# Kernel optimization log

Hardware: AMD Instinct MI355X
Metric: run time of the kernel (lower is better)

The kernel has to match this reference:

```python
import jax, jax.numpy as jnp
import numpy as np

D_MODEL = 1024
N_HEADS = 16
D_K = D_MODEL // N_HEADS
SEQ = 2048
BATCH = 2
THETA = 10000.0


def _rope(x, token_positions):
    # x: [b, h, s, dk]; token_positions: [s] int
    k = jnp.arange(0, D_K, 2, dtype=jnp.float32)
    freqs = 1.0 / (THETA ** (k / D_K))                    # [dk/2]
    angles = token_positions.astype(jnp.float32)[:, None] * freqs[None, :]  # [s, dk/2]
    cos = jnp.cos(angles)
    sin = jnp.sin(angles)
    x1 = x[..., 0::2]
    x2 = x[..., 1::2]
    r1 = x1 * cos - x2 * sin
    r2 = x1 * sin + x2 * cos
    out = jnp.stack([r1, r2], axis=-1)                    # [b,h,s,dk/2,2]
    return out.reshape(x.shape)


def setup_inputs() -> dict:
    key = jax.random.key(0)
    ks = jax.random.split(key, 5)
    sigma = np.sqrt(2.0 / (D_MODEL + D_MODEL))
    x = jax.random.normal(ks[0], (BATCH, SEQ, D_MODEL), dtype=jnp.float32)
    Wq = jax.random.truncated_normal(ks[1], -3.0, 3.0, (D_MODEL, D_MODEL), dtype=jnp.float32) * sigma
    Wk = jax.random.truncated_normal(ks[2], -3.0, 3.0, (D_MODEL, D_MODEL), dtype=jnp.float32) * sigma
    Wv = jax.random.truncated_normal(ks[3], -3.0, 3.0, (D_MODEL, D_MODEL), dtype=jnp.float32) * sigma
    Wo = jax.random.truncated_normal(ks[4], -3.0, 3.0, (D_MODEL, D_MODEL), dtype=jnp.float32) * sigma
    token_positions = jnp.arange(SEQ, dtype=jnp.int64)
    return {"x": x, "Wq": Wq, "Wk": Wk, "Wv": Wv, "Wo": Wo, "token_positions": token_positions}


def reference(x, Wq, Wk, Wv, Wo, token_positions):
    b, s, d = x.shape
    # projections: Linear stores weight [out,in], applies x @ W.T
    Q = x @ Wq.T
    K = x @ Wk.T
    V = x @ Wv.T
    # [b, s, h*dk] -> [b, h, s, dk]
    def split_heads(t):
        return t.reshape(b, s, N_HEADS, D_K).transpose(0, 2, 1, 3)
    Q, K, V = split_heads(Q), split_heads(K), split_heads(V)
    Q = _rope(Q, token_positions)
    K = _rope(K, token_positions)
    scale = 1.0 / np.sqrt(D_K).astype(np.float32)
    scores = jnp.einsum('bhqd,bhkd->bhqk', Q, K) * scale   # [b,h,s,s]
    causal = jnp.tril(jnp.ones((s, s), dtype=bool))
    scores = jnp.where(causal, scores, -jnp.inf)
    attn = jax.nn.softmax(scores, axis=-1)
    out = jnp.einsum('bhqk,bhkd->bhqd', attn, V)           # [b,h,s,dk]
    out = out.transpose(0, 2, 1, 3).reshape(b, s, d)
    return out @ Wo.T
```

## Files before the change

kernel.cpp:

```cpp
#include <hip/hip_runtime.h>
#include <hip/hip_bf16.h>
#include <stdint.h>

#define SEQL   2048
#define NBATCH 2
#define BSZ    4096
#define DMODEL 1024
#define NH     16
#define DK     64
#define NBH    32
#define NCHUNK_TOT 40

typedef __attribute__((ext_vector_type(8)))  short short8;
typedef __attribute__((ext_vector_type(4)))  short shortx4;
typedef __attribute__((ext_vector_type(4)))  float f32x4;
typedef __attribute__((ext_vector_type(16))) float f32x16;
typedef __attribute__((ext_vector_type(4)))  unsigned uint4v;
union PU { uint4v u; short8 s; };

__device__ __forceinline__ short f2b(float f) {
  unsigned u = __float_as_uint(f);
  u = (u + 0x7FFF + ((u >> 16) & 1)) >> 16;
  return (short)u;
}
__device__ __forceinline__ float b2f(short s) {
  return __uint_as_float(((unsigned)(unsigned short)s) << 16);
}
__device__ __forceinline__ unsigned cvtpk(float lo, float hi) {
  unsigned r;
  asm("v_cvt_pk_bf16_f32 %0, %1, %2" : "=v"(r) : "v"(lo), "v"(hi));
  return r;
}
#define PLSWAP(a_, b_) asm("v_permlane32_swap_b32 %0, %1" : "+v"(a_), "+v"(b_))

__device__ __forceinline__ void g2l16(const void* g, void* l) {
  __builtin_amdgcn_global_load_lds(
      (__attribute__((address_space(1))) void*)(uintptr_t)g,
      (__attribute__((address_space(3))) void*)l, 16, 0, 0);
}

__device__ __forceinline__ f32x4 mfma16(short8 a, short8 b, f32x4 c) {
  return __builtin_amdgcn_mfma_f32_16x16x32_bf16(a, b, c, 0, 0, 0);
}
__device__ __forceinline__ f32x16 mfma32(short8 a, short8 b, f32x16 c) {
  return __builtin_amdgcn_mfma_f32_32x32x16_bf16(a, b, c, 0, 0, 0);
}

__global__ void cvt_all(const float* __restrict__ x,  const float* __restrict__ wq,
                        const float* __restrict__ wk, const float* __restrict__ wv,
                        const float* __restrict__ wo, short* __restrict__ xb,
                        short* __restrict__ wqkv, short* __restrict__ wob) {
  long idx = ((long)blockIdx.x * 256 + threadIdx.x) * 4;
  const float* s; short* d; long off;
  if (idx < 4194304L)      { s = x;  d = xb;             off = idx; }
  else if (idx < 5242880L) { s = wq; d = wqkv;           off = idx - 4194304L; }
  else if (idx < 6291456L) { s = wk; d = wqkv + 1048576; off = idx - 5242880L; }
  else if (idx < 7340032L) { s = wv; d = wqkv + 2097152; off = idx - 6291456L; }
  else                     { s = wo; d = wob;            off = idx - 7340032L; }
  float4 v = *(const float4*)(s + off);
  shortx4 r;
  r[0] = f2b(v.x); r[1] = f2b(v.y); r[2] = f2b(v.z); r[3] = f2b(v.w);
  *(shortx4*)(d + off) = r;
}

__global__ __launch_bounds__(512, 1)
void gemm256(const short* __restrict__ A, const short* __restrict__ B,
             short* __restrict__ C) {
  __shared__ short As[2][2][8192];
  __shared__ short Bs[2][2][8192];
  int id = blockIdx.x;
  int swz = (id & 7) * 24 + (id >> 3);
  int bm = swz / 12, bn = swz % 12;
  int brow = bm << 8, bcol = bn << 8;
  int tid = threadIdx.x, w = tid >> 6, l = tid & 63;
  int wm = w >> 2, wn = w & 3;
  int lr = l & 15, lg = l >> 4;
  const short* Abase = A + (long)brow * 1024;
  const short* Bbase = B + (long)bcol * 1024;

  f32x4 acc[8][4];
#pragma unroll
  for (int mi = 0; mi < 8; ++mi)
#pragma unroll
    for (int ni = 0; ni < 4; ++ni) acc[mi][ni] = (f32x4){0.f, 0.f, 0.f, 0.f};

#define STGH(srcbase_, kt_, dst_) do {                                          \
    _Pragma("unroll")                                                           \
    for (int i_ = 0; i_ < 2; ++i_) {                                            \
      int idx_ = i_ * 512 + tid;                                                \
      int r_ = idx_ >> 3, gch_ = (idx_ & 7) ^ (r_ & 7);                         \
      g2l16((srcbase_) + (long)r_ * 1024 + (kt_) * 64 + gch_ * 8,               \
            &(dst_)[idx_ * 8]);                                                 \
    } } while (0)

  STGH(Abase,          0, As[0][0]); STGH(Abase + 131072, 0, As[0][1]);
  STGH(Bbase,          0, Bs[0][0]); STGH(Bbase + 131072, 0, Bs[0][1]);
  STGH(Abase,          1, As[1][0]); STGH(Abase + 131072, 1, As[1][1]);
  STGH(Bbase,          1, Bs[1][0]); STGH(Bbase + 131072, 1, Bs[1][1]);
  asm volatile("s_waitcnt vmcnt(8)" ::: "memory");
  __builtin_amdgcn_s_barrier();

  int brw = (wn & 1) * 64;
  for (int kt = 0; kt < 16; ++kt) {
    int cur = kt & 1;
    const short* Ah = &As[cur][wm][0];
    const short* Bh = &Bs[cur][wn >> 1][0];
    short8 a0[4][2], a1[4][2], bf[4][2];
#pragma unroll
    for (int mi = 0; mi < 4; ++mi)
#pragma unroll
      for (int ks = 0; ks < 2; ++ks)
        a0[mi][ks] = *(const short8*)
            &Ah[(mi * 16 + lr) * 64 + (((ks * 4 + lg) ^ (lr & 7)) << 3)];
#pragma unroll
    for (int ni = 0; ni < 4; ++ni)
#pragma unroll
      for (int ks = 0; ks < 2; ++ks)
        bf[ni][ks] = *(const short8*)
            &Bh[(brw + ni * 16 + lr) * 64 + (((ks * 4 + lg) ^ (lr & 7)) << 3)];
    asm volatile("s_waitcnt lgkmcnt(0)" ::: "memory");
    __builtin_amdgcn_sched_barrier(0);
    __builtin_amdgcn_s_setprio(1);
#pragma unroll
    for (int mi = 0; mi < 4; ++mi)
#pragma unroll
      for (int ni = 0; ni < 2; ++ni)
#pragma unroll
        for (int ks = 0; ks < 2; ++ks)
          acc[mi][ni] = mfma16(a0[mi][ks], bf[ni][ks], acc[mi][ni]);
    __builtin_amdgcn_s_setprio(0);
    __builtin_amdgcn_s_barrier();
#pragma unroll
    for (int mi = 0; mi < 4; ++mi)
#pragma unroll
      for (int ks = 0; ks < 2; ++ks)
        a1[mi][ks] = *(const short8*)
            &Ah[((mi + 4) * 16 + lr) * 64 + (((ks * 4 + lg) ^ (lr & 7)) << 3)];
    __builtin_amdgcn_s_setprio(1);
#pragma unroll
    for (int mi = 0; mi < 4; ++mi)
#pragma unroll
      for (int ni = 2; ni < 4; ++ni)
#pragma unroll
        for (int ks = 0; ks < 2; ++ks)
          acc[mi][ni] = mfma16(a0[mi][ks], bf[ni][ks], acc[mi][ni]);
    __builtin_amdgcn_s_setprio(0);
    asm volatile("s_waitcnt lgkmcnt(0)" ::: "memory");
    __builtin_amdgcn_s_barrier();
    if (kt + 2 < 16) {
      STGH(Abase,          kt + 2, As[cur][0]);
      STGH(Abase + 131072, kt + 2, As[cur][1]);
    }
    __builtin_amdgcn_s_setprio(1);
#pragma unroll
    for (int mi = 0; mi < 4; ++mi)
#pragma unroll
      for (int ni = 0; ni < 2; ++ni)
#pragma unroll
        for (int ks = 0; ks < 2; ++ks)
          acc[mi + 4][ni] = mfma16(a1[mi][ks], bf[ni][ks], acc[mi + 4][ni]);
    __builtin_amdgcn_s_setprio(0);
    __builtin_amdgcn_s_barrier();
    if (kt + 2 < 16) {
      STGH(Bbase,          kt + 2, Bs[cur][0]);
      STGH(Bbase + 131072, kt + 2, Bs[cur][1]);
    }
    __builtin_amdgcn_s_setprio(1);
#pragma unroll
    for (int mi = 0; mi < 4; ++mi)
#pragma unroll
      for (int ni = 2; ni < 4; ++ni)
#pragma unroll
        for (int ks = 0; ks < 2; ++ks)
          acc[mi + 4][ni] = mfma16(a1[mi][ks], bf[ni][ks], acc[mi + 4][ni]);
    __builtin_amdgcn_s_setprio(0);
    if (kt + 1 < 16) {
      if (kt + 2 < 16) asm volatile("s_waitcnt vmcnt(8)" ::: "memory");
      else             asm volatile("s_waitcnt vmcnt(0)" ::: "memory");
    }
    __builtin_amdgcn_s_barrier();
  }
#undef STGH

#pragma unroll
  for (int mi = 0; mi < 8; ++mi)
#pragma unroll
    for (int ni = 0; ni < 4; ++ni)
#pragma unroll
      for (int rr = 0; rr < 4; ++rr) {
        int grow = brow + wm * 128 + mi * 16 + lg * 4 + rr;
        int gcol = bcol + wn * 64 + ni * 16 + lr;
        int mat = gcol >> 10, cin = gcol & 1023;
        C[(long)mat * 4194304 + (long)grow * 1024 + cin] = f2b(acc[mi][ni][rr]);
      }
}

template<int CBF16>
__global__ __launch_bounds__(256, 2)
void gemm_bt(const short* __restrict__ A, const short* __restrict__ B,
             void* __restrict__ Cv, int M, int N, int K,
             long bStride, long cStride) {
  __shared__ short As[2][4096];
  __shared__ short Bs[2][4096];
  B += (long)blockIdx.y * bStride;
  int nbn = N >> 7;
  int bm = blockIdx.x / nbn, bn = blockIdx.x % nbn;
  int tid = threadIdx.x, w = tid >> 6, l = tid & 63;
  int wm = w >> 1, wn = w & 1;
  int lr = l & 15, lg = l >> 4;
  int brow = bm << 7, bcol = bn << 7;

  const f32x4 fz = {0.f, 0.f, 0.f, 0.f};
  f32x4 acc[4][4];
#pragma unroll
  for (int xi = 0; xi < 4; ++xi)
#pragma unroll
    for (int yi = 0; yi < 4; ++yi) acc[xi][yi] = fz;

#define GSTAGE(k0_, bi_) do {                                                   \
    _Pragma("unroll")                                                           \
    for (int i_ = 0; i_ < 2; ++i_) {                                            \
      int c_ = w * 2 + i_;                                                      \
      int chunk_ = c_ * 64 + l;                                                 \
      int row_ = chunk_ >> 2, ch_ = chunk_ & 3;                                 \
      int gch_ = ch_ ^ ((row_ >> 1) & 3);                                       \
      g2l16(A + (long)(brow + row_) * K + (k0_) + gch_ * 8, &As[bi_][c_ * 512]);\
      g2l16(B + (long)(bcol + row_) * K + (k0_) + gch_ * 8, &Bs[bi_][c_ * 512]);\
    }                                                                           \
  } while (0)

  GSTAGE(0, 0);
  for (int k0 = 0; k0 < K; k0 += 32) {
    int cb = (k0 >> 5) & 1;
    if (k0 + 32 < K) {
      GSTAGE(k0 + 32, cb ^ 1);
      asm volatile("s_waitcnt vmcnt(4)" ::: "memory");
    } else {
      asm volatile("s_waitcnt vmcnt(0)" ::: "memory");
    }
    __builtin_amdgcn_s_barrier();

    short8 af[4], bfr[4];
#pragma unroll
    for (int xi = 0; xi < 4; ++xi) {
      int ar = wm * 64 + xi * 16 + lr;
      af[xi] = *(const short8*)&As[cb][ar * 32 + ((lg ^ ((ar >> 1) & 3)) << 3)];
      int br = wn * 64 + xi * 16 + lr;
      bfr[xi] = *(const short8*)&Bs[cb][br * 32 + ((lg ^ ((br >> 1) & 3)) << 3)];
    }
    __builtin_amdgcn_s_setprio(1);
#pragma unroll
    for (int xi = 0; xi < 4; ++xi)
#pragma unroll
      for (int yi = 0; yi < 4; ++yi)
        acc[xi][yi] = mfma16(af[xi], bfr[yi], acc[xi][yi]);
    __builtin_amdgcn_s_setprio(0);
    asm volatile("s_waitcnt lgkmcnt(0)" ::: "memory");
    __builtin_amdgcn_s_barrier();
  }
#undef GSTAGE

  if (CBF16) {
    short* Cp = (short*)Cv + (long)blockIdx.y * cStride;
#pragma unroll
    for (int xi = 0; xi < 4; ++xi)
#pragma unroll
      for (int yi = 0; yi < 4; ++yi)
#pragma unroll
        for (int r = 0; r < 4; ++r) {
          int row = brow + wm * 64 + xi * 16 + lg * 4 + r;
          int col = bcol + wn * 64 + yi * 16 + lr;
          Cp[(long)row * N + col] = f2b(acc[xi][yi][r]);
        }
  } else {
    float* Cp = (float*)Cv;
#pragma unroll
    for (int xi = 0; xi < 4; ++xi)
#pragma unroll
      for (int yi = 0; yi < 4; ++yi)
#pragma unroll
        for (int r = 0; r < 4; ++r) {
          int row = brow + wm * 64 + xi * 16 + lg * 4 + r;
          int col = bcol + wn * 64 + yi * 16 + lr;
          Cp[(long)row * N + col] = acc[xi][yi][r];
        }
  }
}

__global__ void rope_split(const short* __restrict__ qkv, const int* __restrict__ tok,
                           short* __restrict__ Qh, short* __restrict__ Kh) {
  int t = blockIdx.x * 256 + threadIdx.x;
  int qd = t & 15, h = (t >> 4) & 15, bs = t >> 8;
  int b = bs >> 11, s = bs & 2047;
  float pos = (float)tok[s];
  long srcoff = (long)bs * 1024 + h * 64 + qd * 4;
  shortx4 q4 = *(const shortx4*)(qkv + srcoff);
  shortx4 k4 = *(const shortx4*)(qkv + 4194304L + srcoff);
  shortx4 qo, ko;
#pragma unroll
  for (int p = 0; p < 2; ++p) {
    int i = qd * 2 + p;
    float freq = exp2f(-(float)i * (13.287712379549449f / 32.0f));
    float ang = pos * freq;
    float sn, cs;
    sincosf(ang, &sn, &cs);
    const float QS = 0.125f * 1.44269504f;
    float x1 = b2f(q4[p * 2]), x2 = b2f(q4[p * 2 + 1]);
    qo[p * 2]     = f2b((x1 * cs - x2 * sn) * QS);
    qo[p * 2 + 1] = f2b((x1 * sn + x2 * cs) * QS);
    float y1 = b2f(k4[p * 2]), y2 = b2f(k4[p * 2 + 1]);
    ko[p * 2]     = f2b(y1 * cs - y2 * sn);
    ko[p * 2 + 1] = f2b(y1 * sn + y2 * cs);
  }
  long outoff = ((long)(b * 16 + h) * 2048 + s) * 64 + qd * 4;
  *(shortx4*)(Qh + outoff) = qo;
  *(shortx4*)(Kh + outoff) = ko;
}

__global__ void vtrans(const short* __restrict__ Vlin, short* __restrict__ Vt) {
  __shared__ short tile[64][72];
  int s0 = blockIdx.x * 64;
  int bh = blockIdx.y;
  int b = bh >> 4, h = bh & 15;
  int t = threadIdx.x;
  int r = t >> 2, c0 = (t & 3) * 16;
  const short* src = Vlin + ((long)(b * 2048 + s0 + r)) * 1024 + h * 64 + c0;
  *(short8*)&tile[r][c0]     = *(const short8*)src;
  *(short8*)&tile[r][c0 + 8] = *(const short8*)(src + 8);
  __syncthreads();
  int d = t >> 2, sc0 = (t & 3) * 16;
  short8 o0, o1;
#pragma unroll
  for (int j = 0; j < 8; ++j) { o0[j] = tile[sc0 + j][d]; o1[j] = tile[sc0 + 8 + j][d]; }
  short* dst = Vt + ((long)(bh * 64 + d)) * 2048 + s0 + sc0;
  *(short8*)dst       = o0;
  *(short8*)(dst + 8) = o1;
}

__global__ __launch_bounds__(256, 3)
void attn_fwd(const short* __restrict__ Qh, const short* __restrict__ Kh,
              const short* __restrict__ Vt, short* __restrict__ poO,
              float* __restrict__ pmb, float* __restrict__ plb) {
  __shared__ short Ks[3][4096];
  __shared__ short Vs[3][4096];
  int bh = blockIdx.x;
  int xr = 39 - blockIdx.y;
  int qi, c = xr, nc = 1;
  for (qi = 0; qi < 16; ++qi) { nc = (qi >> 2) + 1; if (c < nc) break; c -= nc; }
  int n = 2 * qi + 2;
  int t0 = (c * n) / nc, t1 = ((c + 1) * n) / nc;
  int q0b = qi << 7;
  int tid = threadIdx.x, w = tid >> 6, l = tid & 63;
  int ql = l & 31, hi = l >> 5;
  const short* Qb = Qh + (long)bh * (2048 * 64);
  const short* Kb = Kh + (long)bh * (2048 * 64);
  const short* Vb = Vt + (long)bh * (64 * 2048);
  int qw = q0b + 32 * w;
  int qg = qw + ql;
  int pid = bh * NCHUNK_TOT + xr;

  short8 qf[4];
#pragma unroll
  for (int kc = 0; kc < 4; ++kc)
    qf[kc] = *(const short8*)(Qb + (long)qg * 64 + kc * 16 + hi * 8);

  f32x16 o0, o1;
#pragma unroll
  for (int r = 0; r < 16; ++r) { o0[r] = 0.f; o1[r] = 0.f; }
  float m = -1e30f, lsum = 0.f;

#define STAGE(t_, bufi_) do {                                                   \
    int s0_ = (t_) << 6;                                                        \
    _Pragma("unroll")                                                           \
    for (int i_ = 0; i_ < 2; ++i_) {                                            \
      int c_ = w + 4 * i_;                                                      \
      int g_ = c_ >> 2, cc_ = c_ & 3;                                           \
      g2l16(Kb + ((long)(s0_ + g_ * 32 + ql)) * 64 + cc_ * 16 + hi * 8,         \
            &Ks[bufi_][c_ * 512]);                                              \
      g2l16(Vb + ((long)(g_ * 32 + ql)) * 2048 + s0_ + cc_ * 16 + hi * 8,       \
            &Vs[bufi_][c_ * 512]);                                              \
    }                                                                           \
  } while (0)

  STAGE(t0, 0);
  if (t0 + 1 < t1) STAGE(t0 + 1, 1);
  int cur = 0;

  for (int t = t0; t < t1; ++t) {
    if (t + 2 < t1) {
      int nb = cur + 2; if (nb >= 3) nb -= 3;
      STAGE(t + 2, nb);
      asm volatile("s_waitcnt vmcnt(8)" ::: "memory");
    } else if (t + 1 < t1) {
      asm volatile("s_waitcnt vmcnt(4)" ::: "memory");
    } else {
      asm volatile("s_waitcnt vmcnt(0)" ::: "memory");
    }
    __builtin_amdgcn_s_barrier();
    int s0 = t << 6;
    if (s0 <= qw + 31) {
      bool upper = (s0 + 32 <= qw + 31);
      f32x16 sT0, sT1;
#pragma unroll
      for (int r = 0; r < 16; ++r) { sT0[r] = 0.f; sT1[r] = 0.f; }
      __builtin_amdgcn_s_setprio(1);
#pragma unroll
      for (int kc = 0; kc < 4; ++kc) {
        short8 k0 = *(const short8*)&Ks[cur][(kc * 64 + l) * 8];
        sT0 = mfma32(k0, qf[kc], sT0);
      }
      if (upper) {
#pragma unroll
        for (int kc = 0; kc < 4; ++kc) {
          short8 k1 = *(const short8*)&Ks[cur][((4 + kc) * 64 + l) * 8];
          sT1 = mfma32(k1, qf[kc], sT1);
        }
      }
      __builtin_amdgcn_s_setprio(0);
      if (s0 + 63 > qw) {
#pragma unroll
        for (int r = 0; r < 16; ++r) {
          int kvl = (r & 3) + 8 * (r >> 2) + 4 * hi;
          if (s0 + kvl > qg) sT0[r] = -1e30f;
        }
        if (upper) {
#pragma unroll
          for (int r = 0; r < 16; ++r) {
            int kvl = (r & 3) + 8 * (r >> 2) + 4 * hi;
            if (s0 + 32 + kvl > qg) sT1[r] = -1e30f;
          }
        }
      }
      float pmax = sT0[0];
#pragma unroll
      for (int r = 1; r < 16; ++r) pmax = fmaxf(pmax, sT0[r]);
      if (upper) {
#pragma unroll
        for (int r = 0; r < 16; ++r) pmax = fmaxf(pmax, sT1[r]);
      }
      pmax = fmaxf(pmax, __shfl_xor(pmax, 32));
      if (__any(pmax > m + 11.5416f)) {
        float mn = fmaxf(m, pmax);
        float sf = exp2f(m - mn);
        m = mn;
        lsum *= sf;
#pragma unroll
        for (int r = 0; r < 16; ++r) {
          int row = (r & 3) + 8 * (r >> 2) + 4 * hi;
          float fo = __shfl(sf, row);
          o0[r] *= fo; o1[r] *= fo;
        }
      }
      float rs = 0.f;
#pragma unroll
      for (int r = 0; r < 16; ++r) {
        float p = exp2f(sT0[r] - m);
        sT0[r] = p; rs += p;
      }
      if (upper) {
#pragma unroll
        for (int r = 0; r < 16; ++r) {
          float p = exp2f(sT1[r] - m);
          sT1[r] = p; rs += p;
        }
      }
      rs += __shfl_xor(rs, 32);
      lsum += rs;
      short8 pa[4];
      {
        unsigned cA[4], cB[4];
#pragma unroll
        for (int g = 0; g < 4; ++g) {
          cA[g] = cvtpk(sT0[4 * g], sT0[4 * g + 1]);
          cB[g] = cvtpk(sT0[4 * g + 2], sT0[4 * g + 3]);
        }
        PLSWAP(cA[0], cA[1]); PLSWAP(cB[0], cB[1]);
        PLSWAP(cA[2], cA[3]); PLSWAP(cB[2], cB[3]);
        PU p0; p0.u = (uint4v){cA[0], cB[0], cA[1], cB[1]}; pa[0] = p0.s;
        PU p1; p1.u = (uint4v){cA[2], cB[2], cA[3], cB[3]}; pa[1] = p1.s;
      }
      if (upper) {
        unsigned cA[4], cB[4];
#pragma unroll
        for (int g = 0; g < 4; ++g) {
          cA[g] = cvtpk(sT1[4 * g], sT1[4 * g + 1]);
          cB[g] = cvtpk(sT1[4 * g + 2], sT1[4 * g + 3]);
        }
        PLSWAP(cA[0], cA[1]); PLSWAP(cB[0], cB[1]);
        PLSWAP(cA[2], cA[3]); PLSWAP(cB[2], cB[3]);
        PU p2; p2.u = (uint4v){cA[0], cB[0], cA[1], cB[1]}; pa[2] = p2.s;
        PU p3; p3.u = (uint4v){cA[2], cB[2], cA[3], cB[3]}; pa[3] = p3.s;
      }
      __builtin_amdgcn_s_setprio(1);
#pragma unroll
      for (int kc = 0; kc < 2; ++kc) {
        short8 v0 = *(const short8*)&Vs[cur][(kc * 64 + l) * 8];
        short8 v1 = *(const short8*)&Vs[cur][((4 + kc) * 64 + l) * 8];
        o0 = mfma32(pa[kc], v0, o0);
        o1 = mfma32(pa[kc], v1, o1);
      }
      if (upper) {
#pragma unroll
        for (int kc = 2; kc < 4; ++kc) {
          short8 v0 = *(const short8*)&Vs[cur][(kc * 64 + l) * 8];
          short8 v1 = *(const short8*)&Vs[cur][((4 + kc) * 64 + l) * 8];
          o0 = mfma32(pa[kc], v0, o0);
          o1 = mfma32(pa[kc], v1, o1);
        }
      }
      __builtin_amdgcn_s_setprio(0);
    }
    asm volatile("s_waitcnt lgkmcnt(0)" ::: "memory");
    __builtin_amdgcn_s_barrier();
    ++cur; if (cur >= 3) cur -= 3;
  }
#undef STAGE

  if (hi == 0) {
    pmb[pid * 128 + w * 32 + ql] = m;
    plb[pid * 128 + w * 32 + ql] = lsum;
  }
#pragma unroll
  for (int r = 0; r < 16; ++r) {
    int row = (r & 3) + 8 * (r >> 2) + 4 * hi;
    long basep = ((long)pid * 128 + w * 32 + row) * 64;
    poO[basep + ql]      = f2b(o0[r]);
    poO[basep + 32 + ql] = f2b(o1[r]);
  }
}

__global__ void attn_combine(const short* __restrict__ poO,
                             const float* __restrict__ pmb,
                             const float* __restrict__ plb,
                             short* __restrict__ Oh) {
  int x = blockIdx.x, bh = blockIdx.y;
  int qi = x >> 2, sub = x & 3;
  int t = threadIdx.x;
  int r = sub * 32 + (t >> 3);
  int d0 = (t & 7) * 8;
  int nc = (qi >> 2) + 1;
  int prefix = 0;
  for (int j = 0; j < qi; ++j) prefix += (j >> 2) + 1;
  int base = bh * NCHUNK_TOT + prefix;
  float M = -1e30f;
  for (int i = 0; i < nc; ++i)
    M = fmaxf(M, pmb[(base + i) * 128 + r]);
  float acc0 = 0, acc1 = 0, acc2 = 0, acc3 = 0, acc4 = 0, acc5 = 0, acc6 = 0, acc7 = 0;
  float den = 0.f;
  for (int i = 0; i < nc; ++i) {
    float wgt = exp2f(pmb[(base + i) * 128 + r] - M);
    den += wgt * plb[(base + i) * 128 + r];
    short8 ov = *(const short8*)&poO[((long)(base + i) * 128 + r) * 64 + d0];
    acc0 += wgt * b2f(ov[0]); acc1 += wgt * b2f(ov[1]);
    acc2 += wgt * b2f(ov[2]); acc3 += wgt * b2f(ov[3]);
    acc4 += wgt * b2f(ov[4]); acc5 += wgt * b2f(ov[5]);
    acc6 += wgt * b2f(ov[6]); acc7 += wgt * b2f(ov[7]);
  }
  float inv = 1.0f / den;
  int b = bh >> 4, h = bh & 15;
  int s = qi * 128 + r;
  short8 out;
  out[0] = f2b(acc0 * inv); out[1] = f2b(acc1 * inv);
  out[2] = f2b(acc2 * inv); out[3] = f2b(acc3 * inv);
  out[4] = f2b(acc4 * inv); out[5] = f2b(acc5 * inv);
  out[6] = f2b(acc6 * inv); out[7] = f2b(acc7 * inv);
  *(short8*)&Oh[((long)(b * 2048 + s)) * 1024 + h * 64 + d0] = out;
}

extern "C" void kernel_launch(void* const* d_in, const int* in_sizes, int n_in,
                              void* d_out, int out_size, void* d_ws, size_t ws_size,
                              hipStream_t stream) {
  const float* x  = (const float*)d_in[0];
  const float* wq = (const float*)d_in[1];
  const float* wk = (const float*)d_in[2];
  const float* wv = (const float*)d_in[3];
  const float* wo = (const float*)d_in[4];
  const int* tok  = (const int*)d_in[5];

  short* wsp  = (short*)d_ws;
  short* xb   = wsp;
  short* wqkv = xb + 4194304;
  short* wob  = wqkv + 3145728;
  short* qkv  = wob + 1048576;
  short* qh   = qkv + 12582912;
  short* kh   = qh + 4194304;
  short* vt   = kh + 4194304;
  short* oh   = vt + 4194304;

  short* poO = qkv;
  float* pmb = (float*)xb;
  float* plb = pmb + NCHUNK_TOT * NBH * 128;

  (void)in_sizes; (void)n_in; (void)out_size; (void)ws_size;

  cvt_all<<<8192, 256, 0, stream>>>(x, wq, wk, wv, wo, xb, wqkv, wob);
  gemm256<<<192, 512, 0, stream>>>(xb, wqkv, qkv);
  rope_split<<<4096, 256, 0, stream>>>(qkv, tok, qh, kh);
  vtrans<<<dim3(32, 32), 256, 0, stream>>>(qkv + 8388608, vt);
  attn_fwd<<<dim3(32, NCHUNK_TOT), 256, 0, stream>>>(qh, kh, vt, poO, pmb, plb);
  attn_combine<<<dim3(64, 32), 256, 0, stream>>>(poO, pmb, plb, oh);
  gemm_bt<0><<<dim3(256, 1), 256, 0, stream>>>(oh, wob, d_out, 4096, 1024, 1024,
                                               0L, 0L);
}
```

Baseline: 132.7 us.

## Retile QKV GEMM to 256x192 blocks, lighten attention pipelining and row-sum

The QKV projection GEMM moves from 256x256 tiles on 192 blocks to 256x192 tiles on 256 blocks, so every compute unit on the 256-CU part gets a block, with matching changes to the staging and fragment indexing. The attention kernel drops from triple to double buffering of K/V in LDS and raises launch bounds to 4 blocks per CU for more occupancy. It also keeps per-register running sums so the cross-lane row-sum reduction happens once at the end instead of every tile, and uses v_max3 for the row max. The risks are less latency hiding in attention, extra registers for the row sums, and lower per-block arithmetic intensity in the GEMM.

Result: slower. 142.3 us (+7.2%).

```diff
diff --git a/kernel.cpp b/kernel.cpp
--- a/kernel.cpp
+++ b/kernel.cpp
@@ -30,6 +30,11 @@
   unsigned r;
   asm("v_cvt_pk_bf16_f32 %0, %1, %2" : "=v"(r) : "v"(lo), "v"(hi));
   return r;
+}
+__device__ __forceinline__ float max3f(float a, float b, float c) {
+  float d;
+  asm("v_max3_f32 %0, %1, %2, %3" : "=v"(d) : "v"(a), "v"(b), "v"(c));
+  return d;
 }
 #define PLSWAP(a_, b_) asm("v_permlane32_swap_b32 %0, %1" : "+v"(a_), "+v"(b_))
 
@@ -66,58 +71,62 @@
 __global__ __launch_bounds__(512, 1)
 void gemm256(const short* __restrict__ A, const short* __restrict__ B,
              short* __restrict__ C) {
-  __shared__ short As[2][2][8192];
-  __shared__ short Bs[2][2][8192];
+  __shared__ short As[2][16384];
+  __shared__ short Bs[2][12288];
   int id = blockIdx.x;
-  int swz = (id & 7) * 24 + (id >> 3);
-  int bm = swz / 12, bn = swz % 12;
-  int brow = bm << 8, bcol = bn << 8;
-  int tid = threadIdx.x, w = tid >> 6, l = tid & 63;
+  int swz = (id & 7) * 32 + (id >> 3);
+  int bm = swz >> 4, bn = swz & 15;
+  int brow = bm << 8, bcoln = bn * 192;
+  int tid = threadIdx.x, w = tid >> 6;
   int wm = w >> 2, wn = w & 3;
-  int lr = l & 15, lg = l >> 4;
+  int lr = tid & 15, lg = (tid >> 4) & 3;
   const short* Abase = A + (long)brow * 1024;
-  const short* Bbase = B + (long)bcol * 1024;
-
-  f32x4 acc[8][4];
+  const short* Bbase = B + (long)bcoln * 1024;
+
+  f32x4 acc[8][3];
 #pragma unroll
   for (int mi = 0; mi < 8; ++mi)
 #pragma unroll
-    for (int ni = 0; ni < 4; ++ni) acc[mi][ni] = (f32x4){0.f, 0.f, 0.f, 0.f};
-
-#define STGH(srcbase_, kt_, dst_) do {                                          \
-    _Pragma("unroll")                                                           \
-    for (int i_ = 0; i_ < 2; ++i_) {                                            \
-      int idx_ = i_ * 512 + tid;                                                \
-      int r_ = idx_ >> 3, gch_ = (idx_ & 7) ^ (r_ & 7);                         \
-      g2l16((srcbase_) + (long)r_ * 1024 + (kt_) * 64 + gch_ * 8,               \
-            &(dst_)[idx_ * 8]);                                                 \
-    } } while (0)
-
-  STGH(Abase,          0, As[0][0]); STGH(Abase + 131072, 0, As[0][1]);
-  STGH(Bbase,          0, Bs[0][0]); STGH(Bbase + 131072, 0, Bs[0][1]);
-  STGH(Abase,          1, As[1][0]); STGH(Abase + 131072, 1, As[1][1]);
-  STGH(Bbase,          1, Bs[1][0]); STGH(Bbase + 131072, 1, Bs[1][1]);
-  asm volatile("s_waitcnt vmcnt(8)" ::: "memory");
+    for (int ni = 0; ni < 3; ++ni) acc[mi][ni] = (f32x4){0.f, 0.f, 0.f, 0.f};
+
+#define STGA(s_, kt_, buf_) do {                                                \
+    int r_ = tid >> 3, gch_ = (tid & 7) ^ (r_ & 7);                             \
+    g2l16(Abase + (long)((s_) * 64 + r_) * 1024 + (kt_) * 64 + gch_ * 8,        \
+          &As[buf_][(s_) * 4096 + tid * 8]); } while (0)
+#define STGB(s_, kt_, buf_) do {                                                \
+    int r_ = tid >> 3, gch_ = (tid & 7) ^ (r_ & 7);                             \
+    g2l16(Bbase + (long)((s_) * 64 + r_) * 1024 + (kt_) * 64 + gch_ * 8,        \
+          &Bs[buf_][(s_) * 4096 + tid * 8]); } while (0)
+
+  STGA(0,0,0); STGA(1,0,0); STGA(2,0,0); STGA(3,0,0);
+  STGB(0,0,0); STGB(1,0,0); STGB(2,0,0);
+  STGA(0,1,1); STGA(1,1,1); STGA(2,1,1); STGA(3,1,1);
+  STGB(0,1,1); STGB(1,1,1); STGB(2,1,1);
+  asm volatile("s_waitcnt vmcnt(7)" ::: "memory");
   __builtin_amdgcn_s_barrier();
 
-  int brw = (wn & 1) * 64;
   for (int kt = 0; kt < 16; ++kt) {
     int cur = kt & 1;
-    const short* Ah = &As[cur][wm][0];
-    const short* Bh = &Bs[cur][wn >> 1][0];
-    short8 a0[4][2], a1[4][2], bf[4][2];
-#pragma unroll
-    for (int mi = 0; mi < 4; ++mi)
+    const short* Ah = &As[cur][wm * 8192];
+    const short* Bh = &Bs[cur][0];
+    short8 a0[4][2], a1[4][2], bf[3][2];
+#pragma unroll
+    for (int mi = 0; mi < 4; ++mi) {
+      int rin = mi * 16 + lr;
 #pragma unroll
       for (int ks = 0; ks < 2; ++ks)
         a0[mi][ks] = *(const short8*)
-            &Ah[(mi * 16 + lr) * 64 + (((ks * 4 + lg) ^ (lr & 7)) << 3)];
-#pragma unroll
-    for (int ni = 0; ni < 4; ++ni)
+            &Ah[rin * 64 + (((ks * 4 + lg) ^ (rin & 7)) << 3)];
+    }
+#pragma unroll
+    for (int ni = 0; ni < 3; ++ni) {
+      int ci = wn * 48 + ni * 16 + lr;
+      int sub = ci >> 6, rin = ci & 63;
 #pragma unroll
       for (int ks = 0; ks < 2; ++ks)
         bf[ni][ks] = *(const short8*)
-            &Bh[(brw + ni * 16 + lr) * 64 + (((ks * 4 + lg) ^ (lr & 7)) << 3)];
+            &Bh[sub * 4096 + rin * 64 + (((ks * 4 + lg) ^ (rin & 7)) << 3)];
+    }
     asm volatile("s_waitcnt lgkmcnt(0)" ::: "memory");
     __builtin_amdgcn_sched_barrier(0);
     __builtin_amdgcn_s_setprio(1);
@@ -131,25 +140,26 @@
     __builtin_amdgcn_s_setprio(0);
     __builtin_amdgcn_s_barrier();
 #pragma unroll
-    for (int mi = 0; mi < 4; ++mi)
+    for (int mi = 0; mi < 4; ++mi) {
+      int rin = mi * 16 + lr;
 #pragma unroll
       for (int ks = 0; ks < 2; ++ks)
         a1[mi][ks] = *(const short8*)
-            &Ah[((mi + 4) * 16 + lr) * 64 + (((ks * 4 + lg) ^ (lr & 7)) << 3)];
+            &Ah[4096 + rin * 64 + (((ks * 4 + lg) ^ (rin & 7)) << 3)];
+    }
     __builtin_amdgcn_s_setprio(1);
 #pragma unroll
     for (int mi = 0; mi < 4; ++mi)
 #pragma unroll
-      for (int ni = 2; ni < 4; ++ni)
-#pragma unroll
-        for (int ks = 0; ks < 2; ++ks)
-          acc[mi][ni] = mfma16(a0[mi][ks], bf[ni][ks], acc[mi][ni]);
+      for (int ks = 0; ks < 2; ++ks)
+        acc[mi][2] = mfma16(a0[mi][ks], bf[2][ks], acc[mi][2]);
     __builtin_amdgcn_s_setprio(0);
     asm volatile("s_waitcnt lgkmcnt(0)" ::: "memory");
+    __builtin_amdgcn_sched_barrier(0);
     __builtin_amdgcn_s_barrier();
     if (kt + 2 < 16) {
-      STGH(Abase,          kt + 2, As[cur][0]);
-      STGH(Abase + 131072, kt + 2, As[cur][1]);
+      STGA(0, kt + 2, cur); STGA(1, kt + 2, cur);
+      STGA(2, kt + 2, cur); STGA(3, kt + 2, cur);
     }
     __builtin_amdgcn_s_setprio(1);
 #pragma unroll
@@ -162,34 +172,32 @@
     __builtin_amdgcn_s_setprio(0);
     __builtin_amdgcn_s_barrier();
     if (kt + 2 < 16) {
-      STGH(Bbase,          kt + 2, Bs[cur][0]);
-      STGH(Bbase + 131072, kt + 2, Bs[cur][1]);
+      STGB(0, kt + 2, cur); STGB(1, kt + 2, cur); STGB(2, kt + 2, cur);
     }
     __builtin_amdgcn_s_setprio(1);
 #pragma unroll
     for (int mi = 0; mi < 4; ++mi)
 #pragma unroll
-      for (int ni = 2; ni < 4; ++ni)
-#pragma unroll
-        for (int ks = 0; ks < 2; ++ks)
-          acc[mi + 4][ni] = mfma16(a1[mi][ks], bf[ni][ks], acc[mi + 4][ni]);
+      for (int ks = 0; ks < 2; ++ks)
+        acc[mi + 4][2] = mfma16(a1[mi][ks], bf[2][ks], acc[mi + 4][2]);
     __builtin_amdgcn_s_setprio(0);
     if (kt + 1 < 16) {
-      if (kt + 2 < 16) asm volatile("s_waitcnt vmcnt(8)" ::: "memory");
+      if (kt + 2 < 16) asm volatile("s_waitcnt vmcnt(7)" ::: "memory");
       else             asm volatile("s_waitcnt vmcnt(0)" ::: "memory");
     }
     __builtin_amdgcn_s_barrier();
   }
-#undef STGH
+#undef STGA
+#undef STGB
 
 #pragma unroll
   for (int mi = 0; mi < 8; ++mi)
 #pragma unroll
-    for (int ni = 0; ni < 4; ++ni)
+    for (int ni = 0; ni < 3; ++ni)
 #pragma unroll
       for (int rr = 0; rr < 4; ++rr) {
         int grow = brow + wm * 128 + mi * 16 + lg * 4 + rr;
-        int gcol = bcol + wn * 64 + ni * 16 + lr;
+        int gcol = bcoln + wn * 48 + ni * 16 + lr;
         int mat = gcol >> 10, cin = gcol & 1023;
         C[(long)mat * 4194304 + (long)grow * 1024 + cin] = f2b(acc[mi][ni][rr]);
       }
@@ -337,12 +345,12 @@
   *(short8*)(dst + 8) = o1;
 }
 
-__global__ __launch_bounds__(256, 3)
+__global__ __launch_bounds__(256, 4)
 void attn_fwd(const short* __restrict__ Qh, const short* __restrict__ Kh,
               const short* __restrict__ Vt, short* __restrict__ poO,
               float* __restrict__ pmb, float* __restrict__ plb) {
-  __shared__ short Ks[3][4096];
-  __shared__ short Vs[3][4096];
+  __shared__ short Ks[2][4096];
+  __shared__ short Vs[2][4096];
   int bh = blockIdx.x;
   int xr = 39 - blockIdx.y;
   int qi, c = xr, nc = 1;
@@ -364,10 +372,10 @@
   for (int kc = 0; kc < 4; ++kc)
     qf[kc] = *(const short8*)(Qb + (long)qg * 64 + kc * 16 + hi * 8);
 
-  f32x16 o0, o1;
-#pragma unroll
-  for (int r = 0; r < 16; ++r) { o0[r] = 0.f; o1[r] = 0.f; }
-  float m = -1e30f, lsum = 0.f;
+  f32x16 o0, o1, rsv;
+#pragma unroll
+  for (int r = 0; r < 16; ++r) { o0[r] = 0.f; o1[r] = 0.f; rsv[r] = 0.f; }
+  float m = -1e30f;
 
 #define STAGE(t_, bufi_) do {                                                   \
     int s0_ = (t_) << 6;                                                        \
@@ -383,15 +391,11 @@
   } while (0)
 
   STAGE(t0, 0);
-  if (t0 + 1 < t1) STAGE(t0 + 1, 1);
-  int cur = 0;
 
   for (int t = t0; t < t1; ++t) {
-    if (t + 2 < t1) {
-      int nb = cur + 2; if (nb >= 3) nb -= 3;
-      STAGE(t + 2, nb);
-      asm volatile("s_waitcnt vmcnt(8)" ::: "memory");
-    } else if (t + 1 < t1) {
+    int cur = (t - t0) & 1;
+    if (t + 1 < t1) {
+      STAGE(t + 1, cur ^ 1);
       asm volatile("s_waitcnt vmcnt(4)" ::: "memory");
     } else {
       asm volatile("s_waitcnt vmcnt(0)" ::: "memory");
@@ -431,19 +435,20 @@
           }
         }
       }
-      float pmax = sT0[0];
-#pragma unroll
-      for (int r = 1; r < 16; ++r) pmax = fmaxf(pmax, sT0[r]);
+      float pmax = fmaxf(sT0[0], sT0[1]);
+#pragma unroll
+      for (int r = 2; r < 16; r += 2) pmax = max3f(pmax, sT0[r], sT0[r + 1]);
       if (upper) {
 #pragma unroll
-        for (int r = 0; r < 16; ++r) pmax = fmaxf(pmax, sT1[r]);
+        for (int r = 0; r < 16; r += 2) pmax = max3f(pmax, sT1[r], sT1[r + 1]);
       }
       pmax = fmaxf(pmax, __shfl_xor(pmax, 32));
       if (__any(pmax > m + 11.5416f)) {
         float mn = fmaxf(m, pmax);
         float sf = exp2f(m - mn);
         m = mn;
-        lsum *= sf;
+#pragma unroll
+        for (int r = 0; r < 16; ++r) rsv[r] *= sf;
 #pragma unroll
         for (int r = 0; r < 16; ++r) {
           int row = (r & 3) + 8 * (r >> 2) + 4 * hi;
@@ -451,21 +456,18 @@
           o0[r] *= fo; o1[r] *= fo;
         }
       }
-      float rs = 0.f;
 #pragma unroll
       for (int r = 0; r < 16; ++r) {
         float p = exp2f(sT0[r] - m);
-        sT0[r] = p; rs += p;
+        sT0[r] = p; rsv[r] += p;
       }
       if (upper) {
 #pragma unroll
         for (int r = 0; r < 16; ++r) {
           float p = exp2f(sT1[r] - m);
-          sT1[r] = p; rs += p;
-        }
-      }
-      rs += __shfl_xor(rs, 32);
-      lsum += rs;
+          sT1[r] = p; rsv[r] += p;
+        }
+      }
       short8 pa[4];
       {
         unsigned cA[4], cB[4];
@@ -512,9 +514,13 @@
     }
     asm volatile("s_waitcnt lgkmcnt(0)" ::: "memory");
     __builtin_amdgcn_s_barrier();
-    ++cur; if (cur >= 3) cur -= 3;
   }
 #undef STAGE
+
+  float lsum = 0.f;
+#pragma unroll
+  for (int r = 0; r < 16; ++r) lsum += rsv[r];
+  lsum += __shfl_xor(lsum, 32);
 
   if (hi == 0) {
     pmb[pid * 128 + w * 32 + ql] = m;
@@ -594,7 +600,7 @@
   (void)in_sizes; (void)n_in; (void)out_size; (void)ws_size;
 
   cvt_all<<<8192, 256, 0, stream>>>(x, wq, wk, wv, wo, xb, wqkv, wob);
-  gemm256<<<192, 512, 0, stream>>>(xb, wqkv, qkv);
+  gemm256<<<256, 512, 0, stream>>>(xb, wqkv, qkv);
   rope_split<<<4096, 256, 0, stream>>>(qkv, tok, qh, kh);
   vtrans<<<dim3(32, 32), 256, 0, stream>>>(qkv + 8388608, vt);
   attn_fwd<<<dim3(32, NCHUNK_TOT), 256, 0, stream>>>(qh, kh, vt, poO, pmb, plb);
```
